# Performance work log

Hardware: AMD Instinct MI355X
Metric: run time of the kernel (lower is better)

## Reference

```python
import jax, jax.numpy as jnp
import numpy as np
from jax import lax

NC = 10        # tess_size
EPS = 1e-07


def cpab_basis(nc):
    # Constraint matrix L @ Avees = 0, Avees = [a0,b0,a1,b1,...] per cell.
    # Continuity at interior knots x_i = i/nc, plus zero-boundary v(0)=v(1)=0.
    L = np.zeros((nc + 1, 2 * nc))
    for i in range(1, nc):
        xi = i / nc
        L[i - 1, 2 * (i - 1):2 * i] = [xi, 1.0]
        L[i - 1, 2 * i:2 * i + 2] = [-xi, -1.0]
    L[nc - 1, 1] = 1.0                      # v(0) = b_0 = 0
    L[nc, 2 * nc - 2:2 * nc] = [1.0, 1.0]   # v(1) = a_{nc-1} + b_{nc-1} = 0
    U, S, Vh = np.linalg.svd(L)
    rank = int((S > 1e-8 * S[0]).sum())
    return np.ascontiguousarray(Vh[rank:].T).astype(np.float32)  # (2*nc, nc-1)


def mlp(x1, W0, b0, W1, b1, W2, b2, W3, b3):
    h = jax.nn.relu(x1 @ W0 + b0)
    h = jax.nn.relu(h @ W1 + b1)
    h = jax.nn.relu(h @ W2 + b2)
    return h @ W3 + b3


def integrate_cpab(x, A, nc):
    # x: [N] in (0,1); A: [N, nc, 2] per-cell (slope a, intercept b).
    # Closed-form integration of dphi/dt = a_c*phi + b_c for t in [0,1],
    # walking across cells. Also accumulates s = integral of a(phi(t)) dt,
    # so dphi/dx = exp(s)  (space gradient of the transform).
    a_all = A[..., 0]
    b_all = A[..., 1]
    fnc = jnp.asarray(nc, x.dtype)
    c0 = jnp.clip(jnp.floor(x * nc).astype(jnp.int32), 0, nc - 1)

    def step(carry, _):
        phi, c, t, s, done = carry
        a = jnp.take_along_axis(a_all, c[:, None], 1)[:, 0]
        b = jnp.take_along_axis(b_all, c[:, None], 1)[:, 0]
        v = a * phi + b
        big = jnp.abs(a) > 1e-10
        a_safe = jnp.where(big, a, 1.0)
        # closed-form solution with remaining time t
        psi = jnp.where(big, (phi + b / a_safe) * jnp.exp(a * t) - b / a_safe,
                        phi + b * t)
        lo = c.astype(x.dtype) / fnc
        hi = (c + 1).astype(x.dtype) / fnc
        inside = (psi >= lo) & (psi <= hi)
        xc = jnp.where(v >= 0, hi, lo)          # boundary hit in flow direction
        vb = a * xc + b
        v_safe = jnp.where(v == 0, 1.0, v)
        ratio = jnp.maximum(vb / v_safe, 1e-30)
        t_hit = jnp.where(big, jnp.log(ratio) / a_safe, (xc - phi) / v_safe)
        act = ~done
        cross = act & ~inside
        s = s + jnp.where(act, a * jnp.where(inside, t, t_hit), 0.0)
        phi = jnp.where(cross, xc, jnp.where(act & inside, psi, phi))
        t = jnp.where(cross, t - t_hit, t)
        c = jnp.clip(jnp.where(cross, c + jnp.where(v >= 0, 1, -1), c), 0, nc - 1)
        done = done | inside
        return (phi, c, t, s, done), None

    init = (x, c0, jnp.ones_like(x), jnp.zeros_like(x),
            jnp.zeros(x.shape, bool))
    (phi, _, _, s, _), _ = lax.scan(step, init, None, length=nc + 1)
    return phi, jnp.exp(s)


def _forward(x, B, W0, b0, W1, b1, W2, b2, W3, b3):
    mask = jnp.array([1, 0])  # left=True
    x = jnp.clip(x, EPS, 1.0 - EPS)
    xm = x[:, mask]
    x1, x2 = xm[:, :1], xm[:, 1:]          # [N,1] each
    theta = mlp(x1, W0, b0, W1, b1, W2, b2, W3, b3)   # [N, nc-1]
    A = (theta @ B.T).reshape(-1, NC, 2)    # per-cell (a, b)
    z2, dz2 = integrate_cpab(x2[:, 0], A, NC)
    z = jnp.column_stack([x1[:, 0], z2])[:, mask]
    log_dz_dx = jnp.column_stack([jnp.zeros_like(x1[:, 0]),
                                  jnp.log(dz2)])[:, mask]
    return z, log_dz_dx


def setup_inputs() -> dict:
    key = jax.random.key(0)
    ks = jax.random.split(key, 9)
    N, H, D = 4_194_304, 10, NC - 1
    x = jax.random.uniform(ks[0], (N, 2), jnp.float32)
    sc = 0.5
    return {
        'x': x,
        'B': jnp.asarray(cpab_basis(NC)),
        'W0': jax.random.normal(ks[1], (1, H), jnp.float32) * sc,
        'b0': jax.random.normal(ks[2], (H,), jnp.float32) * 0.1,
        'W1': jax.random.normal(ks[3], (H, H), jnp.float32) * sc,
        'b1': jax.random.normal(ks[4], (H,), jnp.float32) * 0.1,
        'W2': jax.random.normal(ks[5], (H, H), jnp.float32) * sc,
        'b2': jax.random.normal(ks[6], (H,), jnp.float32) * 0.1,
        'W3': jax.random.normal(ks[7], (H, D), jnp.float32) * sc,
        'b3': jax.random.normal(ks[8], (D,), jnp.float32) * 0.1,
    }


def reference(x, B, W0, b0, W1, b1, W2, b2, W3, b3):
    return _forward(x, B, W0, b0, W1, b1, W2, b2, W3, b3)
```

## Files before the change

kernel.cpp:

```cpp
#include <hip/hip_runtime.h>
#include <math.h>

#define NCELL 10
#define TPTS  512
#define BLK   1024

__device__ __forceinline__ float satf(float v) {
    return fminf(fmaxf(v, -3.389e38f), 3.389e38f);
}

__global__ __launch_bounds__(256) void table_kernel(
    const float* __restrict__ B,
    const float* __restrict__ W0, const float* __restrict__ b0,
    const float* __restrict__ W1, const float* __restrict__ b1,
    const float* __restrict__ W2, const float* __restrict__ b2,
    const float* __restrict__ W3, const float* __restrict__ b3,
    float* __restrict__ tab, float lo, float hi, float dx)
{
    const int i = blockIdx.x * 256 + threadIdx.x;
    if (i >= TPTS) return;
    float x1 = fmaf((float)i, dx, lo);
    if (i == TPTS - 1) x1 = hi;

    float h0[10], h1[10], h2[10];
    #pragma unroll
    for (int j = 0; j < 10; ++j)
        h0[j] = fmaxf(fmaf(x1, W0[j], b0[j]), 0.0f);
    #pragma unroll
    for (int j = 0; j < 10; ++j) {
        float acc = b1[j];
        #pragma unroll
        for (int k = 0; k < 10; ++k) acc = fmaf(h0[k], W1[k * 10 + j], acc);
        h1[j] = fmaxf(acc, 0.0f);
    }
    #pragma unroll
    for (int j = 0; j < 10; ++j) {
        float acc = b2[j];
        #pragma unroll
        for (int k = 0; k < 10; ++k) acc = fmaf(h1[k], W2[k * 10 + j], acc);
        h2[j] = fmaxf(acc, 0.0f);
    }
    float theta[9];
    #pragma unroll
    for (int j = 0; j < 9; ++j) {
        float acc = b3[j];
        #pragma unroll
        for (int k = 0; k < 10; ++k) acc = fmaf(h2[k], W3[k * 9 + j], acc);
        theta[j] = acc;
    }
    #pragma unroll
    for (int j = 1; j <= 9; ++j) {
        float aj = 0.f, bj = 0.f;
        #pragma unroll
        for (int q = 0; q < 9; ++q) {
            aj = fmaf(theta[q], B[(2 * j) * 9 + q], aj);
            bj = fmaf(theta[q], B[(2 * j + 1) * 9 + q], bj);
        }
        tab[(j - 1) * TPTS + i] = fmaf(aj, (float)j / 10.0f, bj);
    }
}

__global__ __launch_bounds__(BLK) void cpab_kernel(
    const float* __restrict__ x,
    const float* __restrict__ tab,
    float* __restrict__ out, int N,
    float lo, float inv_dx)
{
    __shared__ float sT[9 * TPTS];

    const int tid = threadIdx.x;

    {
        const float4* g4 = reinterpret_cast<const float4*>(tab);
        float4* s4 = reinterpret_cast<float4*>(sT);
        #pragma unroll
        for (int k = tid; k < 9 * TPTS / 4; k += BLK) s4[k] = g4[k];
    }
    __syncthreads();

    const int i = blockIdx.x * BLK + tid;
    if (i >= N) return;

    const float2 xv = reinterpret_cast<const float2*>(x)[i];
    const float hi_clip = 1.0f - 1e-7f;
    const float x2 = fminf(fmaxf(xv.x, 1e-7f), hi_clip);
    const float x1 = fminf(fmaxf(xv.y, 1e-7f), hi_clip);

    const float tt  = (x1 - lo) * inv_dx;
    const int  cell = min((int)tt, TPTS - 2);
    const float f   = tt - (float)cell;

    const float* base = sT + cell;
    auto node = [&](int j) -> float {
        const int jj = (min(max(j, 1), 9) - 1) * TPTS;
        const float v0 = base[jj];
        const float v1 = base[jj + 1];
        const float v  = fmaf(f, v1 - v0, v0);
        return (j >= 1 && j <= 9) ? v : 0.0f;
    };

    const float p10  = x2 * 10.0f;
    const int   cc0  = (int)p10;
    const float frac = p10 - (float)cc0;
    const float nc = node(cc0);
    const float nn = node(cc0 + 1);
    const float a0s = (nn - nc) * 10.0f;
    const float u0 = fmaf(nn - nc, frac, nc);
    const bool  right = (u0 >= 0.0f);
    const float d10   = right ? 10.0f : -10.0f;
    const int   dint  = right ? 1 : -1;

    float p  = x2;
    float u  = u0;
    float ru = __builtin_amdgcn_rcpf(u0);
    int   cn = cc0 + (right ? 1 : 0);
    float w  = right ? nn : nc;
    float t  = 1.0f;
    float a  = 0.0f, ra = 1.0f;
    bool  big = false;

    #pragma unroll 1
    for (int it = 0; ; ++it) {
        a   = (w - u) * d10;
        big = fabsf(a) > 1e-10f;
        ra  = __builtin_amdgcn_rcpf(big ? a : 1.0f);
        const float q  = w * ru;
        const float lg = __logf(q);
        const float xc = (float)cn * 0.1f;
        const float t_hit = big ? (lg * ra) : ((xc - p) * ru);
        if (!(t_hit < t) || it >= 11) break;
        t  -= t_hit;
        p   = xc;
        u   = w;
        ru  = __builtin_amdgcn_rcpf(w);
        cn += dint;
        w   = node(cn);
    }

    const float e   = __expf(a * t);
    float phi = big ? fmaf(u * ra, e - 1.0f, p) : fmaf(u, t, p);
    const float ru0 = __builtin_amdgcn_rcpf(u0);
    float ldz = __logf(fabsf(u * e * ru0));
    if (u0 == 0.0f) { phi = x2; ldz = a0s; }

    reinterpret_cast<float2*>(out)[i] = make_float2(satf(phi), x1);
    reinterpret_cast<float2*>(out + (size_t)2 * N)[i] = make_float2(satf(ldz), 0.0f);
}

extern "C" void kernel_launch(void* const* d_in, const int* in_sizes, int n_in,
                              void* d_out, int out_size, void* d_ws, size_t ws_size,
                              hipStream_t stream) {
    (void)n_in; (void)out_size; (void)ws_size;
    const float* x  = (const float*)d_in[0];
    const float* B  = (const float*)d_in[1];
    const float* W0 = (const float*)d_in[2];
    const float* b0 = (const float*)d_in[3];
    const float* W1 = (const float*)d_in[4];
    const float* b1 = (const float*)d_in[5];
    const float* W2 = (const float*)d_in[6];
    const float* b2 = (const float*)d_in[7];
    const float* W3 = (const float*)d_in[8];
    const float* b3 = (const float*)d_in[9];
    float* ws  = (float*)d_ws;
    float* out = (float*)d_out;

    const int N = in_sizes[0] / 2;
    const float lo = 1e-7f, hi = 1.0f - 1e-7f;
    const float dx = (hi - lo) / (float)(TPTS - 1);
    const float inv_dx = (float)(TPTS - 1) / (hi - lo);

    table_kernel<<<(TPTS + 255) / 256, 256, 0, stream>>>(
        B, W0, b0, W1, b1, W2, b2, W3, b3, ws, lo, hi, dx);
    cpab_kernel<<<(N + BLK - 1) / BLK, BLK, 0, stream>>>(
        x, ws, out, N, lo, inv_dx);
}
```

Baseline: 122.1 us.

## Replace data-dependent cell-walk loop with fully unrolled predicated sweep

The early-exit loop over cells is replaced by a fixed ten-step unrolled sweep. All node values along the flow direction are prefetched up front, and the active state is tracked with predicates rather than a branch. This removes wavefront divergence and serialized shared-memory latency in the walk, at the cost of always doing the log/rcp work for every step. The block size is also halved to 512.

```diff
diff --git a/kernel.cpp b/kernel.cpp
--- a/kernel.cpp
+++ b/kernel.cpp
@@ -3,7 +3,7 @@
 
 #define NCELL 10
 #define TPTS  512
-#define BLK   1024
+#define BLK   512
 
 __device__ __forceinline__ float satf(float v) {
     return fminf(fmaxf(v, -3.389e38f), 3.389e38f);
@@ -96,7 +96,7 @@
         const float v0 = base[jj];
         const float v1 = base[jj + 1];
         const float v  = fmaf(f, v1 - v0, v0);
-        return (j >= 1 && j <= 9) ? v : 0.0f;
+        return ((unsigned)(j - 1) < 9u) ? v : 0.0f;
     };
 
     const float p10  = x2 * 10.0f;
@@ -109,38 +109,47 @@
     const bool  right = (u0 >= 0.0f);
     const float d10   = right ? 10.0f : -10.0f;
     const int   dint  = right ? 1 : -1;
+    const int   cn0   = cc0 + (right ? 1 : 0);
 
-    float p  = x2;
-    float u  = u0;
-    float ru = __builtin_amdgcn_rcpf(u0);
-    int   cn = cc0 + (right ? 1 : 0);
-    float w  = right ? nn : nc;
-    float t  = 1.0f;
-    float a  = 0.0f, ra = 1.0f;
-    bool  big = false;
+    float w[10];
+    #pragma unroll
+    for (int k = 0; k < 10; ++k) w[k] = node(cn0 + k * dint);
 
-    #pragma unroll 1
-    for (int it = 0; ; ++it) {
-        a   = (w - u) * d10;
-        big = fabsf(a) > 1e-10f;
-        ra  = __builtin_amdgcn_rcpf(big ? a : 1.0f);
-        const float q  = w * ru;
-        const float lg = __logf(q);
-        const float xc = (float)cn * 0.1f;
-        const float t_hit = big ? (lg * ra) : ((xc - p) * ru);
-        if (!(t_hit < t) || it >= 11) break;
-        t  -= t_hit;
-        p   = xc;
-        u   = w;
-        ru  = __builtin_amdgcn_rcpf(w);
-        cn += dint;
-        w   = node(cn);
+    const float ru0 = __builtin_amdgcn_rcpf(u0);
+
+    float trem = 1.0f;
+    float fa = 0.0f, fu = u0, fp = x2;
+    bool  act = true;
+
+    #pragma unroll
+    for (int k = 0; k < 10; ++k) {
+        const float u_in  = (k == 0) ? u0  : w[k - 1];
+        const float ru_in = (k == 0) ? ru0 : __builtin_amdgcn_rcpf(w[k - 1]);
+        const float p_in  = (k == 0) ? x2  : (float)(cn0 + (k - 1) * dint) * 0.1f;
+        const float a_k   = (w[k] - u_in) * d10;
+
+        fa = act ? a_k  : fa;
+        fu = act ? u_in : fu;
+        fp = act ? p_in : fp;
+
+        if (k < 9) {
+            const bool  big_k = fabsf(a_k) > 1e-10f;
+            const float ra_k  = __builtin_amdgcn_rcpf(big_k ? a_k : 1.0f);
+            const float xc_k  = (float)(cn0 + k * dint) * 0.1f;
+            const float q_k   = w[k] * ru_in;
+            const float lg    = __logf(q_k);
+            const float th    = big_k ? lg * ra_k : (xc_k - p_in) * ru_in;
+            const bool cross = act && (th < trem);
+            trem = cross ? (trem - th) : trem;
+            act  = cross;
+        }
     }
 
-    const float e   = __expf(a * t);
-    float phi = big ? fmaf(u * ra, e - 1.0f, p) : fmaf(u, t, p);
-    const float ru0 = __builtin_amdgcn_rcpf(u0);
-    float ldz = __logf(fabsf(u * e * ru0));
+    const bool  fbig = fabsf(fa) > 1e-10f;
+    const float fra  = __builtin_amdgcn_rcpf(fbig ? fa : 1.0f);
+    const float e    = __expf(fa * trem);
+    float phi = fbig ? fmaf(fu * fra, e - 1.0f, fp) : fmaf(fu, trem, fp);
+    float ldz = __logf(fabsf(fu * e * ru0));
     if (u0 == 0.0f) { phi = x2; ldz = a0s; }
 
     reinterpret_cast<float2*>(out)[i] = make_float2(satf(phi), x1);
```

After: 140.9 us. +15.4%, slower.

## Precompute cumulative cell-crossing times and use a branchless prefix search with a grid-stride loop

Applied to the files above, without the earlier changes.

The table kernel now also precomputes, for every grid point of x1, the cumulative crossing times through each cell in both flow directions. The main kernel uses these prefix sums to find the final cell with a fixed, unrolled 9-step comparison instead of a data-dependent loop with a log and a reciprocal per step. The main kernel also switches to a persistent grid-stride launch of 512 blocks, so the larger shared table (35 columns with zero padding) is loaded once per block rather than once per 1024 points. The cost is more shared memory per block, which may lower occupancy, and possible precision differences from interpolating the cumulative times in x1.

```diff
diff --git a/kernel.cpp b/kernel.cpp
--- a/kernel.cpp
+++ b/kernel.cpp
@@ -4,6 +4,11 @@
 #define NCELL 10
 #define TPTS  512
 #define BLK   1024
+#define GRID  512
+#define NCOLS 13
+#define PRCOL 13
+#define PLCOL 24
+#define TCOLS 35
 
 __device__ __forceinline__ float satf(float v) {
     return fminf(fmaxf(v, -3.389e38f), 3.389e38f);
@@ -11,7 +16,7 @@
 
 __global__ __launch_bounds__(256) void table_kernel(
     const float* __restrict__ B,
-    const float* __restrict__ W0, const float* __restrict__ b0,
+    const float* __restrict__ W0, const float* __restrict__ b0v,
     const float* __restrict__ W1, const float* __restrict__ b1,
     const float* __restrict__ W2, const float* __restrict__ b2,
     const float* __restrict__ W3, const float* __restrict__ b3,
@@ -25,7 +30,7 @@
     float h0[10], h1[10], h2[10];
     #pragma unroll
     for (int j = 0; j < 10; ++j)
-        h0[j] = fmaxf(fmaf(x1, W0[j], b0[j]), 0.0f);
+        h0[j] = fmaxf(fmaf(x1, W0[j], b0v[j]), 0.0f);
     #pragma unroll
     for (int j = 0; j < 10; ++j) {
         float acc = b1[j];
@@ -48,6 +53,8 @@
         for (int k = 0; k < 10; ++k) acc = fmaf(h2[k], W3[k * 9 + j], acc);
         theta[j] = acc;
     }
+    float n[11];
+    n[0] = 0.0f; n[10] = 0.0f;
     #pragma unroll
     for (int j = 1; j <= 9; ++j) {
         float aj = 0.f, bj = 0.f;
@@ -56,7 +63,25 @@
             aj = fmaf(theta[q], B[(2 * j) * 9 + q], aj);
             bj = fmaf(theta[q], B[(2 * j + 1) * 9 + q], bj);
         }
-        tab[(j - 1) * TPTS + i] = fmaf(aj, (float)j / 10.0f, bj);
+        n[j] = fmaf(aj, (float)j / 10.0f, bj);
+        tab[(j - 1) * TPTS + i] = n[j];
+    }
+
+    float accR = 0.0f, accL = 0.0f;
+    tab[9 * TPTS + i]  = 0.0f;
+    tab[20 * TPTS + i] = 0.0f;
+    #pragma unroll
+    for (int c = 0; c < 10; ++c) {
+        const float a = 10.0f * (n[c + 1] - n[c]);
+        const bool big = fabsf(a) > 1e-10f;
+        const float tr = big ? (__logf(n[c + 1] / n[c]) / a) : (0.1f / n[c]);
+        const float tl = big ? (__logf(n[c] / n[c + 1]) / a) : (-0.1f / n[c + 1]);
+        const float er = (tr != tr) ? 2.0f : fminf(fmaxf(tr, -2.0f), 2.0f);
+        const float el = (tl != tl) ? 2.0f : fminf(fmaxf(tl, -2.0f), 2.0f);
+        accR += er;
+        accL -= el;
+        tab[(9 + 1 + c) * TPTS + i]  = accR;
+        tab[(20 + 1 + c) * TPTS + i] = accL;
     }
 }
 
@@ -66,85 +91,112 @@
     float* __restrict__ out, int N,
     float lo, float inv_dx)
 {
-    __shared__ float sT[9 * TPTS];
+    __shared__ float sT[TCOLS * TPTS];
 
     const int tid = threadIdx.x;
 
     {
         const float4* g4 = reinterpret_cast<const float4*>(tab);
         float4* s4 = reinterpret_cast<float4*>(sT);
-        #pragma unroll
-        for (int k = tid; k < 9 * TPTS / 4; k += BLK) s4[k] = g4[k];
+        #pragma unroll 1
+        for (int k = tid; k < TCOLS * TPTS / 4; k += BLK) {
+            const int col = k >> 7;
+            const int win = k & 127;
+            float4 v = make_float4(0.f, 0.f, 0.f, 0.f);
+            if (col >= 2 && col <= 10)
+                v = g4[(col - 2) * 128 + win];
+            else if (col >= PRCOL && col <= PRCOL + 10)
+                v = g4[(9 + (col - PRCOL)) * 128 + win];
+            else if (col >= PLCOL && col <= PLCOL + 10)
+                v = g4[(20 + (col - PLCOL)) * 128 + win];
+            s4[k] = v;
+        }
     }
     __syncthreads();
 
-    const int i = blockIdx.x * BLK + tid;
-    if (i >= N) return;
-
-    const float2 xv = reinterpret_cast<const float2*>(x)[i];
     const float hi_clip = 1.0f - 1e-7f;
-    const float x2 = fminf(fmaxf(xv.x, 1e-7f), hi_clip);
-    const float x1 = fminf(fmaxf(xv.y, 1e-7f), hi_clip);
-
-    const float tt  = (x1 - lo) * inv_dx;
-    const int  cell = min((int)tt, TPTS - 2);
-    const float f   = tt - (float)cell;
-
-    const float* base = sT + cell;
-    auto node = [&](int j) -> float {
-        const int jj = (min(max(j, 1), 9) - 1) * TPTS;
-        const float v0 = base[jj];
-        const float v1 = base[jj + 1];
-        const float v  = fmaf(f, v1 - v0, v0);
-        return (j >= 1 && j <= 9) ? v : 0.0f;
-    };
-
-    const float p10  = x2 * 10.0f;
-    const int   cc0  = (int)p10;
-    const float frac = p10 - (float)cc0;
-    const float nc = node(cc0);
-    const float nn = node(cc0 + 1);
-    const float a0s = (nn - nc) * 10.0f;
-    const float u0 = fmaf(nn - nc, frac, nc);
-    const bool  right = (u0 >= 0.0f);
-    const float d10   = right ? 10.0f : -10.0f;
-    const int   dint  = right ? 1 : -1;
-
-    float p  = x2;
-    float u  = u0;
-    float ru = __builtin_amdgcn_rcpf(u0);
-    int   cn = cc0 + (right ? 1 : 0);
-    float w  = right ? nn : nc;
-    float t  = 1.0f;
-    float a  = 0.0f, ra = 1.0f;
-    bool  big = false;
-
-    #pragma unroll 1
-    for (int it = 0; ; ++it) {
-        a   = (w - u) * d10;
-        big = fabsf(a) > 1e-10f;
-        ra  = __builtin_amdgcn_rcpf(big ? a : 1.0f);
-        const float q  = w * ru;
-        const float lg = __logf(q);
-        const float xc = (float)cn * 0.1f;
-        const float t_hit = big ? (lg * ra) : ((xc - p) * ru);
-        if (!(t_hit < t) || it >= 11) break;
-        t  -= t_hit;
-        p   = xc;
-        u   = w;
-        ru  = __builtin_amdgcn_rcpf(w);
-        cn += dint;
-        w   = node(cn);
-    }
-
-    const float e   = __expf(a * t);
-    float phi = big ? fmaf(u * ra, e - 1.0f, p) : fmaf(u, t, p);
-    const float ru0 = __builtin_amdgcn_rcpf(u0);
-    float ldz = __logf(fabsf(u * e * ru0));
-    if (u0 == 0.0f) { phi = x2; ldz = a0s; }
-
-    reinterpret_cast<float2*>(out)[i] = make_float2(satf(phi), x1);
-    reinterpret_cast<float2*>(out + (size_t)2 * N)[i] = make_float2(satf(ldz), 0.0f);
+
+    for (int i = blockIdx.x * BLK + tid; i < N; i += GRID * BLK) {
+        const float2 xv = reinterpret_cast<const float2*>(x)[i];
+        const float x2 = fminf(fmaxf(xv.x, 1e-7f), hi_clip);
+        const float x1 = fminf(fmaxf(xv.y, 1e-7f), hi_clip);
+
+        const float tt  = (x1 - lo) * inv_dx;
+        const int  cell = min((int)tt, TPTS - 2);
+        const float f   = tt - (float)cell;
+
+        const float* nodeB = sT + cell;
+        auto node = [&](int j) -> float {
+            const float* pp = nodeB + (j + 1) * TPTS;
+            return fmaf(f, pp[1] - pp[0], pp[0]);
+        };
+        auto plerp = [&](const float* Pb, int e) -> float {
+            const float* pp = Pb + e * TPTS;
+            return fmaf(f, pp[1] - pp[0], pp[0]);
+        };
+
+        const float p10  = x2 * 10.0f;
+        const int   cc0  = (int)p10;
+        const float frac = p10 - (float)cc0;
+        const float nc = node(cc0);
+        const float nn = node(cc0 + 1);
+        const float a0s = (nn - nc) * 10.0f;
+        const float u0 = fmaf(nn - nc, frac, nc);
+        const bool  right = (u0 >= 0.0f);
+        const float d10   = right ? 10.0f : -10.0f;
+        const int   dint  = right ? 1 : -1;
+        const int   b0    = cc0 + (right ? 1 : 0);
+
+        const float ru0 = __builtin_amdgcn_rcpf(u0);
+        const float w0  = right ? nn : nc;
+        const float a0  = (w0 - u0) * d10;
+        const bool  big0 = fabsf(a0) > 1e-10f;
+        const float ra0  = __builtin_amdgcn_rcpf(big0 ? a0 : 1.0f);
+        const float q0   = w0 * ru0;
+        const float lg0  = __logf(q0);
+        const float xc0  = (float)b0 * 0.1f;
+        const float th0  = big0 ? (lg0 * ra0) : ((xc0 - x2) * ru0);
+        const bool  crossA = (th0 < 1.0f);
+        const float t1 = crossA ? 1.0f - th0 : 1.0f;
+
+        const float* Pb = sT + (right ? PRCOL : PLCOL) * TPTS + cell;
+        const float Pb0 = plerp(Pb, b0);
+        bool  cr  = crossA;
+        float t_f = t1;
+        int   m   = 0;
+        int   e   = b0;
+        #pragma unroll
+        for (int k = 1; k <= 9; ++k) {
+            e += dint;
+            const int ec = min(max(e, 0), 10);
+            const float S = plerp(Pb, ec) - Pb0;
+            cr = cr && (S < t1);
+            t_f = cr ? (t1 - S) : t_f;
+            m  += cr ? 1 : 0;
+        }
+
+        int je = b0 + (right ? m : -m);
+        je = min(max(je, 0), 10);
+        const float uf = node(je);
+        const float wf = node(je + dint);
+        const float af = (wf - uf) * d10;
+
+        const float Ua = crossA ? uf : u0;
+        const float Aa = crossA ? af : a0;
+        const float Pa = crossA ? (float)je * 0.1f : x2;
+        const float Ta = crossA ? t_f : 1.0f;
+
+        const bool  bigf = fabsf(Aa) > 1e-10f;
+        const float raf  = __builtin_amdgcn_rcpf(bigf ? Aa : 1.0f);
+        const float ee   = __expf(Aa * Ta);
+        float phi = bigf ? fmaf(Ua * raf, ee - 1.0f, Pa) : fmaf(Ua, Ta, Pa);
+        float ldz = __logf(fabsf(Ua * ee * ru0));
+        if (u0 == 0.0f) { phi = x2; ldz = a0s; }
+
+        reinterpret_cast<float2*>(out)[i] = make_float2(satf(phi), x1);
+        reinterpret_cast<float2*>(out + (size_t)2 * N)[i] =
+            make_float2(satf(ldz), 0.0f);
+    }
 }
 
 extern "C" void kernel_launch(void* const* d_in, const int* in_sizes, int n_in,
@@ -171,6 +223,6 @@
 
     table_kernel<<<(TPTS + 255) / 256, 256, 0, stream>>>(
         B, W0, b0, W1, b1, W2, b2, W3, b3, ws, lo, hi, dx);
-    cpab_kernel<<<(N + BLK - 1) / BLK, BLK, 0, stream>>>(
+    cpab_kernel<<<GRID, BLK, 0, stream>>>(
         x, ws, out, N, lo, inv_dx);
 }
```

Measured after the change: 136.5 us. +11.8%, slower.
